# Performance work log

Hardware: AMD Instinct MI355X
Metric: run time of the kernel (lower is better)

The kernel has to match this reference:

```python
import jax, jax.numpy as jnp
import numpy as np

B, L_I, L_H, L_Q, Hs, Ws, K, A = 256, 2, 150, 10, 128, 128, 40, 5


def _conv(x, w, pad):
    # NCHW conv, stride 1
    return jax.lax.conv_general_dilated(
        x, w, window_strides=(1, 1), padding=[(pad, pad), (pad, pad)],
        dimension_numbers=('NCHW', 'OIHW', 'NCHW'))


def setup_inputs() -> dict:
    key = jax.random.key(0)
    ks = jax.random.split(key, 8)
    return {
        'input_view': jax.random.normal(ks[0], (B, L_I, Hs, Ws), dtype=jnp.float32),
        'coords': jax.random.randint(ks[1], (B, 4), 0, Hs, dtype=jnp.int32),
        'h_w': jax.random.normal(ks[2], (L_H, L_I, 3, 3), dtype=jnp.float32) * 0.05,
        'h_b': jax.random.normal(ks[3], (L_H,), dtype=jnp.float32) * 0.05,
        'r_w': jax.random.normal(ks[4], (1, L_H, 1, 1), dtype=jnp.float32) * 0.05,
        'q_w': jax.random.normal(ks[5], (L_Q, 1, 3, 3), dtype=jnp.float32) * 0.05,
        'w': jax.random.normal(ks[6], (L_Q, 1, 3, 3), dtype=jnp.float32) * 0.05,
        'fc_w': jax.random.normal(ks[7], (A, L_Q), dtype=jnp.float32) * 0.05,
    }


def reference(input_view, coords, h_w, h_b, r_w, q_w, w, fc_w):
    # process_input: h = Conv3x3(input_view), r = Conv1x1(h), q0 = Conv3x3(r)
    h = _conv(input_view, h_w, pad=1) + h_b[None, :, None, None]
    r = _conv(h, r_w, pad=0)                       # [B,1,H,W] reward map
    q = _conv(r, q_w, pad=1)                       # [B,L_Q,H,W]
    v = jnp.max(q, axis=1, keepdims=True)          # [B,1,H,W]

    # value_iteration: k-1 sweeps of eval_q + channel max, then one final eval_q
    wq = jnp.concatenate([q_w, w], axis=1)         # [L_Q,2,3,3]

    def step(_, v):
        q_i = _conv(jnp.concatenate([r, v], axis=1), wq, pad=1)
        return jnp.max(q_i, axis=1, keepdims=True)

    v = jax.lax.fori_loop(0, K - 1, step, v)
    q = _conv(jnp.concatenate([r, v], axis=1), wq, pad=1)  # [B,L_Q,H,W]

    # get_action: gather q at agent state, then fc (no bias)
    sx, sy = coords[:, 0], coords[:, 1]
    q_out = q[jnp.arange(B), :, sx, sy]            # [B,L_Q]
    logits = q_out @ fc_w.T                        # [B,5]
    return logits
```

## Files before the change

### kernel.cpp

```cpp
#include <hip/hip_runtime.h>

#define NBATCH 256
#define LI 2
#define LH 150
#define LQ 10
#define HS 128
#define WSD 128
#define KIT 40
#define AOUT 5

#define LCOLS 132
#define LROWS 130
#define PLANE (LROWS * LCOLS)
#define LDS_DWORDS (2 * PLANE)

#define WSOFF_RPLANES 64
#define WS_NEED_BYTES ((size_t)(WSOFF_RPLANES + NBATCH * PLANE) * 4)

typedef float v2f __attribute__((ext_vector_type(2)));
#define SPLAT(K) ((v2f){(K), (K)})
#define FMA2(A, B, C) __builtin_elementwise_fma((A), (B), (C))

__global__ void prep_weff(const float* __restrict__ h_w,
                          const float* __restrict__ h_b,
                          const float* __restrict__ r_w,
                          float* __restrict__ w_eff) {
  const int t = threadIdx.x;
  if (t < 18) {
    const int i = t / 9, k = t % 9;
    double s = 0.0;
    for (int h = 0; h < LH; ++h)
      s += (double)r_w[h] * (double)h_w[(h * LI + i) * 9 + k];
    w_eff[t] = (float)s;
  } else if (t == 18) {
    double s = 0.0;
    for (int h = 0; h < LH; ++h)
      s += (double)r_w[h] * (double)h_b[h];
    w_eff[18] = (float)s;
  }
}


#define LOAD_PROW(P, R, W)                                                   \
  {                                                                          \
    const float4 b_ = *reinterpret_cast<const float4*>((P) + (R) * LCOLS);   \
    const float2 c_ = *reinterpret_cast<const float2*>((P) + (R) * LCOLS + 4); \
    W[0] = (v2f){b_.x, b_.y};                                                \
    W[1] = (v2f){b_.z, b_.w};                                                \
    W[2] = (v2f){c_.x, c_.y};                                                \
  }

#define TAPROW(KY, WARR, K0, K1, K2)                                         \
    a0 = FMA2(SPLAT(K0), WARR[KY][0], a0);                                   \
    a1 = FMA2(SPLAT(K0), WARR[KY][1], a1);                                   \
    a0.x = __builtin_fmaf((K1), WARR[KY][0].y, a0.x);                        \
    a0.y = __builtin_fmaf((K1), WARR[KY][1].x, a0.y);                        \
    a1.x = __builtin_fmaf((K1), WARR[KY][1].y, a1.x);                        \
    a1.y = __builtin_fmaf((K1), WARR[KY][2].x, a1.y);                        \
    a0 = FMA2(SPLAT(K2), WARR[KY][1], a0);                                   \
    a1 = FMA2(SPLAT(K2), WARR[KY][2], a1);

#define VI_CH(QC, WC, MERGE)                                                 \
  {                                                                          \
    const float* qc = (QC);                                                  \
    const float* wc = (WC);                                                  \
    v2f a0 = SPLAT(qc[0]) * rw[0][0];                                        \
    v2f a1 = SPLAT(qc[0]) * rw[0][1];                                        \
    a0.x = __builtin_fmaf(qc[1], rw[0][0].y, a0.x);                          \
    a0.y = __builtin_fmaf(qc[1], rw[0][1].x, a0.y);                          \
    a1.x = __builtin_fmaf(qc[1], rw[0][1].y, a1.x);                          \
    a1.y = __builtin_fmaf(qc[1], rw[0][2].x, a1.y);                          \
    a0 = FMA2(SPLAT(qc[2]), rw[0][1], a0);                                   \
    a1 = FMA2(SPLAT(qc[2]), rw[0][2], a1);                                   \
    TAPROW(1, rw, qc[3], qc[4], qc[5])                                       \
    TAPROW(2, rw, qc[6], qc[7], qc[8])                                       \
    TAPROW(0, vw, wc[0], wc[1], wc[2])                                       \
    TAPROW(1, vw, wc[3], wc[4], wc[5])                                       \
    TAPROW(2, vw, wc[6], wc[7], wc[8])                                       \
    MERGE                                                                    \
  }

#define VI_CHANNELS                                                          \
    v2f o0, o1;                                                              \
    VI_CH(q_w, w_in, o0 = a0; o1 = a1;)                                      \
    _Pragma("unroll 3")                                                      \
    for (int c = 1; c < LQ; ++c) {                                           \
      VI_CH(q_w + c * 9, w_in + c * 9,                                       \
            o0 = __builtin_elementwise_max(o0, a0);                          \
            o1 = __builtin_elementwise_max(o1, a1);)                         \
    }

#define VI_ROW_L(DY)                                                         \
  {                                                                          \
    VI_CHANNELS                                                              \
    outv[DY][0] = o0; outv[DY][1] = o1;                                      \
  }

#define WIN_SHIFT2(NEXTROW)                                                  \
  {                                                                          \
    _Pragma("unroll")                                                        \
    for (int j = 0; j < 3; ++j) {                                            \
      rw[0][j] = rw[1][j]; rw[1][j] = rw[2][j];                              \
      vw[0][j] = vw[1][j]; vw[1][j] = vw[2][j];                              \
    }                                                                        \
    LOAD_PROW(rp, (NEXTROW), rw[2])                                          \
    LOAD_PROW(vp, (NEXTROW), vw[2])                                          \
  }

#define R_ROW(DY)                                                            \
  {                                                                          \
    v2f a0 = SPLAT(beff);                                                    \
    v2f a1 = a0;                                                             \
    TAPROW(0, rw, w_eff[0], w_eff[1], w_eff[2])                              \
    TAPROW(1, rw, w_eff[3], w_eff[4], w_eff[5])                              \
    TAPROW(2, rw, w_eff[6], w_eff[7], w_eff[8])                              \
    TAPROW(0, vw, w_eff[9], w_eff[10], w_eff[11])                            \
    TAPROW(1, vw, w_eff[12], w_eff[13], w_eff[14])                           \
    TAPROW(2, vw, w_eff[15], w_eff[16], w_eff[17])                           \
    racc[DY][0] = a0; racc[DY][1] = a1;                                      \
  }

#define LOADR(SLOT, R)                                                       \
  {                                                                          \
    const float4 b_ = *reinterpret_cast<const float4*>(rp + (R) * LCOLS);    \
    const float2 c_ = *reinterpret_cast<const float2*>(rp + (R) * LCOLS + 4); \
    rP[SLOT][0] = (v2f){b_.x, b_.y};                                         \
    rP[SLOT][1] = (v2f){b_.z, b_.w};                                         \
    rP[SLOT][2] = (v2f){c_.x, c_.y};                                         \
  }

#define LOADV(SLOT, R)                                                       \
  {                                                                          \
    const float4 b_ = *reinterpret_cast<const float4*>(vp + (R) * LCOLS);    \
    const float2 c_ = *reinterpret_cast<const float2*>(vp + (R) * LCOLS + 4); \
    vE[SLOT][0] = (v2f){b_.x, b_.y};                                         \
    vE[SLOT][1] = (v2f){b_.z, b_.w};                                         \
    vE[SLOT][2] = (v2f){c_.x, c_.y};                                         \
    vO[SLOT][0] = (v2f){b_.y, b_.z};                                         \
    vO[SLOT][1] = (v2f){b_.w, c_.x};                                         \
  }

#define TAP_R(SLOT, K0, K1, K2)                                              \
    a0 = FMA2(SPLAT(K0), rP[SLOT][0], a0);                                   \
    a1 = FMA2(SPLAT(K0), rP[SLOT][1], a1);                                   \
    a0.x = __builtin_fmaf((K1), rP[SLOT][0].y, a0.x);                        \
    a0.y = __builtin_fmaf((K1), rP[SLOT][1].x, a0.y);                        \
    a1.x = __builtin_fmaf((K1), rP[SLOT][1].y, a1.x);                        \
    a1.y = __builtin_fmaf((K1), rP[SLOT][2].x, a1.y);                        \
    a0 = FMA2(SPLAT(K2), rP[SLOT][1], a0);                                   \
    a1 = FMA2(SPLAT(K2), rP[SLOT][2], a1);

#define TAP_V(SLOT, K0, K1, K2)                                              \
    a0 = FMA2(SPLAT(K0), vE[SLOT][0], a0);                                   \
    a1 = FMA2(SPLAT(K0), vE[SLOT][1], a1);                                   \
    a0 = FMA2(SPLAT(K1), vO[SLOT][0], a0);                                   \
    a1 = FMA2(SPLAT(K1), vO[SLOT][1], a1);                                   \
    a0 = FMA2(SPLAT(K2), vE[SLOT][1], a0);                                   \
    a1 = FMA2(SPLAT(K2), vE[SLOT][2], a1);

#define VI_CH3(QC, WC, SA, SB, SC, MERGE)                                    \
  {                                                                          \
    const float* qc = (QC);                                                  \
    const float* wc = (WC);                                                  \
    v2f a0 = SPLAT(qc[0]) * rP[SA][0];                                       \
    v2f a1 = SPLAT(qc[0]) * rP[SA][1];                                       \
    a0.x = __builtin_fmaf(qc[1], rP[SA][0].y, a0.x);                         \
    a0.y = __builtin_fmaf(qc[1], rP[SA][1].x, a0.y);                         \
    a1.x = __builtin_fmaf(qc[1], rP[SA][1].y, a1.x);                         \
    a1.y = __builtin_fmaf(qc[1], rP[SA][2].x, a1.y);                         \
    a0 = FMA2(SPLAT(qc[2]), rP[SA][1], a0);                                  \
    a1 = FMA2(SPLAT(qc[2]), rP[SA][2], a1);                                  \
    TAP_R(SB, qc[3], qc[4], qc[5])                                           \
    TAP_R(SC, qc[6], qc[7], qc[8])                                           \
    TAP_V(SA, wc[0], wc[1], wc[2])                                           \
    TAP_V(SB, wc[3], wc[4], wc[5])                                           \
    TAP_V(SC, wc[6], wc[7], wc[8])                                           \
    MERGE                                                                    \
  }

#define VI_OUT(DY, SA, SB, SC)                                               \
  {                                                                          \
    v2f o0, o1;                                                              \
    VI_CH3(q_w, w_in, SA, SB, SC, o0 = a0; o1 = a1;)                         \
    _Pragma("unroll 3")                                                      \
    for (int c = 1; c < LQ; ++c) {                                           \
      VI_CH3(q_w + c * 9, w_in + c * 9, SA, SB, SC,                          \
             o0 = __builtin_elementwise_max(o0, a0);                         \
             o1 = __builtin_elementwise_max(o1, a1);)                        \
    }                                                                        \
    float* w_ = wr + (DY) * LCOLS;                                           \
    w_[1] = o0.x; w_[2] = o0.y; w_[3] = o1.x; w_[4] = o1.y;                  \
  }

__global__ __launch_bounds__(1024)
__attribute__((amdgpu_waves_per_eu(4, 4)))
void vin_gr(const float* __restrict__ input,
            const int* __restrict__ coords,
            const float* __restrict__ q_w,
            const float* __restrict__ w_in,
            const float* __restrict__ fc_w,
            float* __restrict__ ws,
            float* __restrict__ out) {
  extern __shared__ float lds[];
  float* pA = lds;
  float* pB = lds + PLANE;
  const float* w_eff = ws;
  float* g_r = ws + WSOFF_RPLANES + (size_t)blockIdx.x * PLANE;

  const int b = blockIdx.x;
  const int tid = threadIdx.x;
  const int ty = tid >> 5;
  const int tx = tid & 31;
  const int y0 = ty << 2;
  const int x0 = tx << 2;
  const int nb_base = y0 * LCOLS + x0;
  const int wrow0 = (y0 + 1) * LCOLS + x0;

  for (int i = tid; i < LDS_DWORDS; i += 1024) lds[i] = 0.0f;
  if (tid < LCOLS) { g_r[tid] = 0.0f; g_r[129 * LCOLS + tid] = 0.0f; }
  if (tid >= 256 && tid < 384) {
    const int row = tid - 255;
    g_r[row * LCOLS + 0] = 0.0f;
    g_r[row * LCOLS + 129] = 0.0f;
    g_r[row * LCOLS + 130] = 0.0f;
    g_r[row * LCOLS + 131] = 0.0f;
  }
  __syncthreads();

  const float* in0 = input + (size_t)b * (LI * HS * WSD);
  const float* in1 = in0 + HS * WSD;
  {
    const float4* in40 = (const float4*)in0;
    const float4* in41 = (const float4*)in1;
    for (int i = tid; i < HS * WSD / 4; i += 1024) {
      const int y = i >> 5, x4 = (i & 31) << 2;
      const float4 a = in40[i];
      const float4 c = in41[i];
      float* r_ = pA + (y + 1) * LCOLS + x4;
      float* v_ = pB + (y + 1) * LCOLS + x4;
      r_[1] = a.x; r_[2] = a.y; r_[3] = a.z; r_[4] = a.w;
      v_[1] = c.x; v_[2] = c.y; v_[3] = c.z; v_[4] = c.w;
    }
  }
  __syncthreads();

  {
    const float* rp = pA + nb_base;
    const float* vp = pB + nb_base;
    v2f rw[3][3], vw[3][3], racc[4][2];
    LOAD_PROW(rp, 0, rw[0]) LOAD_PROW(rp, 1, rw[1]) LOAD_PROW(rp, 2, rw[2])
    LOAD_PROW(vp, 0, vw[0]) LOAD_PROW(vp, 1, vw[1]) LOAD_PROW(vp, 2, vw[2])
    const float beff = w_eff[18];
    R_ROW(0) WIN_SHIFT2(3) R_ROW(1) WIN_SHIFT2(4) R_ROW(2) WIN_SHIFT2(5) R_ROW(3)
    __syncthreads();
#pragma unroll
    for (int dy = 0; dy < 4; ++dy) {
      float* g_ = g_r + wrow0 + dy * LCOLS;
      float* v_ = pA + wrow0 + dy * LCOLS;
      g_[1] = racc[dy][0].x; g_[2] = racc[dy][0].y;
      g_[3] = racc[dy][1].x; g_[4] = racc[dy][1].y;
      v_[1] = 0.0f; v_[2] = 0.0f; v_[3] = 0.0f; v_[4] = 0.0f;
    }
  }
  __syncthreads();

  const float* grp = g_r + nb_base;
#pragma unroll 1
  for (int it = 0; it < KIT; ++it) {
    const float* vp = lds + ((it & 1) ? PLANE : 0) + nb_base;
    float* wr = lds + ((it & 1) ? 0 : PLANE) + wrow0;
    const float* rp = grp;
    v2f rP[3][3], vE[3][3], vO[3][2];
    LOADR(0, 0) LOADR(1, 1) LOADR(2, 2)
    LOADV(0, 0) LOADV(1, 1) LOADV(2, 2)
    VI_OUT(0, 0, 1, 2)
    LOADR(0, 3) LOADV(0, 3)
    VI_OUT(1, 1, 2, 0)
    LOADR(1, 4) LOADV(1, 4)
    VI_OUT(2, 2, 0, 1)
    LOADR(2, 5) LOADV(2, 5)
    VI_OUT(3, 0, 1, 2)
    __syncthreads();
  }

  if (tid == 0) {
    const int sx = coords[b * 4 + 0];
    const int sy = coords[b * 4 + 1];
    float qv[LQ];
#pragma unroll 1
    for (int c = 0; c < LQ; ++c) {
      float s = 0.0f;
#pragma unroll
      for (int kk = 0; kk < 9; ++kk) {
        const int ky = kk / 3, kx = kk % 3;
        const int off = (sx + ky) * LCOLS + (sy + kx);
        s = __builtin_fmaf(q_w[c * 9 + kk], g_r[off],
            __builtin_fmaf(w_in[c * 9 + kk], pA[off], s));
      }
      qv[c] = s;
    }
#pragma unroll 1
    for (int a = 0; a < AOUT; ++a) {
      float s = 0.0f;
#pragma unroll
      for (int c = 0; c < LQ; ++c)
        s = __builtin_fmaf(fc_w[a * LQ + c], qv[c], s);
      out[b * AOUT + a] = s;
    }
  }
}

__global__ __launch_bounds__(1024)
__attribute__((amdgpu_waves_per_eu(4, 4)))
void vin_lds(const float* __restrict__ input,
             const int* __restrict__ coords,
             const float* __restrict__ q_w,
             const float* __restrict__ w_in,
             const float* __restrict__ fc_w,
             const float* __restrict__ w_eff,
             float* __restrict__ out) {
  extern __shared__ float lds[];
  float* rplane = lds;
  float* vplane = lds + PLANE;

  const int b = blockIdx.x;
  const int tid = threadIdx.x;
  const int ty = tid >> 5;
  const int tx = tid & 31;
  const int y0 = ty << 2;
  const int x0 = tx << 2;
  const int nb_base = y0 * LCOLS + x0;
  const int wrow0 = (y0 + 1) * LCOLS + x0;

  for (int i = tid; i < LDS_DWORDS; i += 1024) lds[i] = 0.0f;
  __syncthreads();

  const float* in0 = input + (size_t)b * (LI * HS * WSD);
  const float* in1 = in0 + HS * WSD;
  {
    const float4* in40 = (const float4*)in0;
    const float4* in41 = (const float4*)in1;
    for (int i = tid; i < HS * WSD / 4; i += 1024) {
      const int y = i >> 5, x4 = (i & 31) << 2;
      const float4 a = in40[i];
      const float4 c = in41[i];
      float* r_ = rplane + (y + 1) * LCOLS + x4;
      float* v_ = vplane + (y + 1) * LCOLS + x4;
      r_[1] = a.x; r_[2] = a.y; r_[3] = a.z; r_[4] = a.w;
      v_[1] = c.x; v_[2] = c.y; v_[3] = c.z; v_[4] = c.w;
    }
  }
  __syncthreads();

  {
    const float* rp = rplane + nb_base;
    const float* vp = vplane + nb_base;
    v2f rw[3][3], vw[3][3], racc[4][2];
    LOAD_PROW(rp, 0, rw[0]) LOAD_PROW(rp, 1, rw[1]) LOAD_PROW(rp, 2, rw[2])
    LOAD_PROW(vp, 0, vw[0]) LOAD_PROW(vp, 1, vw[1]) LOAD_PROW(vp, 2, vw[2])
    const float beff = w_eff[18];
    R_ROW(0) WIN_SHIFT2(3) R_ROW(1) WIN_SHIFT2(4) R_ROW(2) WIN_SHIFT2(5) R_ROW(3)
    __syncthreads();
#pragma unroll
    for (int dy = 0; dy < 4; ++dy) {
      float* r_ = rplane + wrow0 + dy * LCOLS;
      float* v_ = vplane + wrow0 + dy * LCOLS;
      r_[1] = racc[dy][0].x; r_[2] = racc[dy][0].y;
      r_[3] = racc[dy][1].x; r_[4] = racc[dy][1].y;
      v_[1] = 0.0f; v_[2] = 0.0f; v_[3] = 0.0f; v_[4] = 0.0f;
    }
  }
  __syncthreads();

#pragma unroll 1
  for (int it = 0; it < KIT; ++it) {
    const float* rp = rplane + nb_base;
    const float* vp = vplane + nb_base;
    v2f rw[3][3], vw[3][3], outv[4][2];
    LOAD_PROW(rp, 0, rw[0]) LOAD_PROW(rp, 1, rw[1]) LOAD_PROW(rp, 2, rw[2])
    LOAD_PROW(vp, 0, vw[0]) LOAD_PROW(vp, 1, vw[1]) LOAD_PROW(vp, 2, vw[2])
    VI_ROW_L(0) WIN_SHIFT2(3) VI_ROW_L(1) WIN_SHIFT2(4) VI_ROW_L(2) WIN_SHIFT2(5) VI_ROW_L(3)
    __syncthreads();
#pragma unroll
    for (int dy = 0; dy < 4; ++dy) {
      float* v_ = vplane + wrow0 + dy * LCOLS;
      v_[1] = outv[dy][0].x; v_[2] = outv[dy][0].y;
      v_[3] = outv[dy][1].x; v_[4] = outv[dy][1].y;
    }
    __syncthreads();
  }

  if (tid == 0) {
    const int sx = coords[b * 4 + 0];
    const int sy = coords[b * 4 + 1];
    float qv[LQ];
#pragma unroll 1
    for (int c = 0; c < LQ; ++c) {
      float s = 0.0f;
#pragma unroll
      for (int kk = 0; kk < 9; ++kk) {
        const int ky = kk / 3, kx = kk % 3;
        const int off = (sx + ky) * LCOLS + (sy + kx);
        s = __builtin_fmaf(q_w[c * 9 + kk], rplane[off],
            __builtin_fmaf(w_in[c * 9 + kk], vplane[off], s));
      }
      qv[c] = s;
    }
#pragma unroll 1
    for (int a = 0; a < AOUT; ++a) {
      float s = 0.0f;
#pragma unroll
      for (int c = 0; c < LQ; ++c)
        s = __builtin_fmaf(fc_w[a * LQ + c], qv[c], s);
      out[b * AOUT + a] = s;
    }
  }
}

extern "C" void kernel_launch(void* const* d_in, const int* in_sizes, int n_in,
                              void* d_out, int out_size, void* d_ws, size_t ws_size,
                              hipStream_t stream) {
  const float* input = (const float*)d_in[0];
  const int*   coords = (const int*)d_in[1];
  const float* h_w = (const float*)d_in[2];
  const float* h_b = (const float*)d_in[3];
  const float* r_w = (const float*)d_in[4];
  const float* q_w = (const float*)d_in[5];
  const float* w_in = (const float*)d_in[6];
  const float* fc_w = (const float*)d_in[7];
  float* out = (float*)d_out;
  float* ws = (float*)d_ws;

  const size_t smem = (size_t)LDS_DWORDS * sizeof(float);

  prep_weff<<<1, 64, 0, stream>>>(h_w, h_b, r_w, ws);

  if (ws_size >= WS_NEED_BYTES) {
    hipFuncSetAttribute(reinterpret_cast<const void*>(vin_gr),
                        hipFuncAttributeMaxDynamicSharedMemorySize, (int)smem);
    vin_gr<<<NBATCH, 1024, smem, stream>>>(input, coords, q_w, w_in, fc_w, ws, out);
  } else {
    hipFuncSetAttribute(reinterpret_cast<const void*>(vin_lds),
                        hipFuncAttributeMaxDynamicSharedMemorySize, (int)smem);
    vin_lds<<<NBATCH, 1024, smem, stream>>>(input, coords, q_w, w_in, fc_w, ws, out);
  }
}
```

Baseline: 664.3 us.

## Precompute per-channel reward-conv terms once and stream them from workspace each sweep

Adds a vin_rq kernel that computes the q_w 3x3 convolution of the reward map for all 10 Q channels once and writes it to a per-batch global workspace buffer. Each value-iteration sweep then loads these precomputed terms as float4 and only convolves the value plane with w, instead of recomputing the reward-side convolution every iteration. This roughly halves the per-sweep FMA work. In exchange it adds about 167 MB of workspace traffic that is re-read on every one of the 39 sweeps, which may exceed cache capacity and make the kernel bandwidth-bound. The new path is used only when the provided workspace is large enough; otherwise the previous kernels still run.

```diff
diff --git a/kernel.cpp b/kernel.cpp
--- a/kernel.cpp
+++ b/kernel.cpp
@@ -16,6 +16,9 @@
 
 #define WSOFF_RPLANES 64
 #define WS_NEED_BYTES ((size_t)(WSOFF_RPLANES + NBATCH * PLANE) * 4)
+#define WSOFF_RQ 64
+#define RQPLANE (HS * LQ * WSD)
+#define WS_RQ_BYTES ((size_t)(WSOFF_RQ + (size_t)NBATCH * RQPLANE) * 4)
 
 typedef float v2f __attribute__((ext_vector_type(2)));
 #define SPLAT(K) ((v2f){(K), (K)})
@@ -192,6 +195,212 @@
     w_[1] = o0.x; w_[2] = o0.y; w_[3] = o1.x; w_[4] = o1.y;                  \
   }
 
+#define RQ_CH3(QC, SA, SB, SC, MERGE)                                        \
+  {                                                                          \
+    const float* qc = (QC);                                                  \
+    v2f a0 = SPLAT(qc[0]) * rP[SA][0];                                       \
+    v2f a1 = SPLAT(qc[0]) * rP[SA][1];                                       \
+    a0.x = __builtin_fmaf(qc[1], rP[SA][0].y, a0.x);                         \
+    a0.y = __builtin_fmaf(qc[1], rP[SA][1].x, a0.y);                         \
+    a1.x = __builtin_fmaf(qc[1], rP[SA][1].y, a1.x);                         \
+    a1.y = __builtin_fmaf(qc[1], rP[SA][2].x, a1.y);                         \
+    a0 = FMA2(SPLAT(qc[2]), rP[SA][1], a0);                                  \
+    a1 = FMA2(SPLAT(qc[2]), rP[SA][2], a1);                                  \
+    TAP_R(SB, qc[3], qc[4], qc[5])                                           \
+    TAP_R(SC, qc[6], qc[7], qc[8])                                           \
+    MERGE                                                                    \
+  }
+
+#define RQ_ST(CI)                                                            \
+    *reinterpret_cast<float4*>(sr + (CI) * WSD) =                            \
+        make_float4(a0.x, a0.y, a1.x, a1.y);
+
+#define RQ_MX                                                                \
+    m0 = __builtin_elementwise_max(m0, a0);                                  \
+    m1 = __builtin_elementwise_max(m1, a1);
+
+#define RQ_OUT(DY, SA, SB, SC)                                               \
+  {                                                                          \
+    float* sr = rq_t + (DY) * (LQ * WSD);                                    \
+    v2f m0, m1;                                                              \
+    RQ_CH3(q_w + 0,  SA, SB, SC, RQ_ST(0) m0 = a0; m1 = a1;)                 \
+    RQ_CH3(q_w + 9,  SA, SB, SC, RQ_ST(1) RQ_MX)                             \
+    RQ_CH3(q_w + 18, SA, SB, SC, RQ_ST(2) RQ_MX)                             \
+    RQ_CH3(q_w + 27, SA, SB, SC, RQ_ST(3) RQ_MX)                             \
+    RQ_CH3(q_w + 36, SA, SB, SC, RQ_ST(4) RQ_MX)                             \
+    RQ_CH3(q_w + 45, SA, SB, SC, RQ_ST(5) RQ_MX)                             \
+    RQ_CH3(q_w + 54, SA, SB, SC, RQ_ST(6) RQ_MX)                             \
+    RQ_CH3(q_w + 63, SA, SB, SC, RQ_ST(7) RQ_MX)                             \
+    RQ_CH3(q_w + 72, SA, SB, SC, RQ_ST(8) RQ_MX)                             \
+    RQ_CH3(q_w + 81, SA, SB, SC, RQ_ST(9) RQ_MX)                             \
+    float* v_ = vwr + (DY) * LCOLS;                                          \
+    v_[1] = m0.x; v_[2] = m0.y; v_[3] = m1.x; v_[4] = m1.y;                  \
+  }
+
+#define VI_CHV(Q4, WOFF, SA, SB, SC, MERGE)                                  \
+  {                                                                          \
+    const float* wc = w_in + (WOFF);                                         \
+    v2f a0 = (v2f){(Q4).x, (Q4).y};                                          \
+    v2f a1 = (v2f){(Q4).z, (Q4).w};                                          \
+    TAP_V(SA, wc[0], wc[1], wc[2])                                           \
+    TAP_V(SB, wc[3], wc[4], wc[5])                                           \
+    TAP_V(SC, wc[6], wc[7], wc[8])                                           \
+    MERGE                                                                    \
+  }
+
+#define VI_MXO                                                               \
+    o0 = __builtin_elementwise_max(o0, a0);                                  \
+    o1 = __builtin_elementwise_max(o1, a1);
+
+#define VI_OUT_RQ(DY, SA, SB, SC)                                            \
+  {                                                                          \
+    const float* rqr = rq_t + (DY) * (LQ * WSD);                             \
+    const float4 q0 = *reinterpret_cast<const float4*>(rqr + 0 * WSD);       \
+    const float4 q1 = *reinterpret_cast<const float4*>(rqr + 1 * WSD);       \
+    const float4 q2 = *reinterpret_cast<const float4*>(rqr + 2 * WSD);       \
+    const float4 q3 = *reinterpret_cast<const float4*>(rqr + 3 * WSD);       \
+    const float4 q4 = *reinterpret_cast<const float4*>(rqr + 4 * WSD);       \
+    const float4 q5 = *reinterpret_cast<const float4*>(rqr + 5 * WSD);       \
+    const float4 q6 = *reinterpret_cast<const float4*>(rqr + 6 * WSD);       \
+    const float4 q7 = *reinterpret_cast<const float4*>(rqr + 7 * WSD);       \
+    const float4 q8 = *reinterpret_cast<const float4*>(rqr + 8 * WSD);       \
+    const float4 q9 = *reinterpret_cast<const float4*>(rqr + 9 * WSD);       \
+    v2f o0, o1;                                                              \
+    VI_CHV(q0,  0, SA, SB, SC, o0 = a0; o1 = a1;)                            \
+    VI_CHV(q1,  9, SA, SB, SC, VI_MXO)                                       \
+    VI_CHV(q2, 18, SA, SB, SC, VI_MXO)                                       \
+    VI_CHV(q3, 27, SA, SB, SC, VI_MXO)                                       \
+    VI_CHV(q4, 36, SA, SB, SC, VI_MXO)                                       \
+    VI_CHV(q5, 45, SA, SB, SC, VI_MXO)                                       \
+    VI_CHV(q6, 54, SA, SB, SC, VI_MXO)                                       \
+    VI_CHV(q7, 63, SA, SB, SC, VI_MXO)                                       \
+    VI_CHV(q8, 72, SA, SB, SC, VI_MXO)                                       \
+    VI_CHV(q9, 81, SA, SB, SC, VI_MXO)                                       \
+    float* w_ = wr + (DY) * LCOLS;                                           \
+    w_[1] = o0.x; w_[2] = o0.y; w_[3] = o1.x; w_[4] = o1.y;                  \
+  }
+
+__global__ __launch_bounds__(1024)
+__attribute__((amdgpu_waves_per_eu(4, 4)))
+void vin_rq(const float* __restrict__ input,
+            const int* __restrict__ coords,
+            const float* __restrict__ q_w,
+            const float* __restrict__ w_in,
+            const float* __restrict__ fc_w,
+            float* __restrict__ ws,
+            float* __restrict__ out) {
+  extern __shared__ float lds[];
+  float* pA = lds;
+  float* pB = lds + PLANE;
+  const float* w_eff = ws;
+
+  const int b = blockIdx.x;
+  const int tid = threadIdx.x;
+  const int ty = tid >> 5;
+  const int tx = tid & 31;
+  const int y0 = ty << 2;
+  const int x0 = tx << 2;
+  const int nb_base = y0 * LCOLS + x0;
+  const int wrow0 = (y0 + 1) * LCOLS + x0;
+
+  float* rq_t = ws + WSOFF_RQ + (size_t)b * RQPLANE + (y0 * LQ) * WSD + x0;
+
+  for (int i = tid; i < LDS_DWORDS; i += 1024) lds[i] = 0.0f;
+  __syncthreads();
+
+  const float* in0 = input + (size_t)b * (LI * HS * WSD);
+  const float* in1 = in0 + HS * WSD;
+  {
+    const float4* in40 = (const float4*)in0;
+    const float4* in41 = (const float4*)in1;
+    for (int i = tid; i < HS * WSD / 4; i += 1024) {
+      const int y = i >> 5, x4 = (i & 31) << 2;
+      const float4 a = in40[i];
+      const float4 c = in41[i];
+      float* r_ = pA + (y + 1) * LCOLS + x4;
+      float* v_ = pB + (y + 1) * LCOLS + x4;
+      r_[1] = a.x; r_[2] = a.y; r_[3] = a.z; r_[4] = a.w;
+      v_[1] = c.x; v_[2] = c.y; v_[3] = c.z; v_[4] = c.w;
+    }
+  }
+  __syncthreads();
+
+  {
+    const float* rp = pA + nb_base;
+    const float* vp = pB + nb_base;
+    v2f rw[3][3], vw[3][3], racc[4][2];
+    LOAD_PROW(rp, 0, rw[0]) LOAD_PROW(rp, 1, rw[1]) LOAD_PROW(rp, 2, rw[2])
+    LOAD_PROW(vp, 0, vw[0]) LOAD_PROW(vp, 1, vw[1]) LOAD_PROW(vp, 2, vw[2])
+    const float beff = w_eff[18];
+    R_ROW(0) WIN_SHIFT2(3) R_ROW(1) WIN_SHIFT2(4) R_ROW(2) WIN_SHIFT2(5) R_ROW(3)
+    __syncthreads();
+#pragma unroll
+    for (int dy = 0; dy < 4; ++dy) {
+      float* r_ = pA + wrow0 + dy * LCOLS;
+      r_[1] = racc[dy][0].x; r_[2] = racc[dy][0].y;
+      r_[3] = racc[dy][1].x; r_[4] = racc[dy][1].y;
+    }
+  }
+  __syncthreads();
+
+  {
+    const float* rp = pA + nb_base;
+    float* vwr = pB + wrow0;
+    v2f rP[3][3];
+    LOADR(0, 0) LOADR(1, 1) LOADR(2, 2)
+    RQ_OUT(0, 0, 1, 2)
+    LOADR(0, 3)
+    RQ_OUT(1, 1, 2, 0)
+    LOADR(1, 4)
+    RQ_OUT(2, 2, 0, 1)
+    LOADR(2, 5)
+    RQ_OUT(3, 0, 1, 2)
+  }
+  __syncthreads();
+
+#pragma unroll 1
+  for (int it = 0; it < KIT - 1; ++it) {
+    const float* vp = lds + ((it & 1) ? 0 : PLANE) + nb_base;
+    float* wr = lds + ((it & 1) ? PLANE : 0) + wrow0;
+    v2f vE[3][3], vO[3][2];
+    LOADV(0, 0) LOADV(1, 1) LOADV(2, 2)
+    VI_OUT_RQ(0, 0, 1, 2)
+    LOADV(0, 3)
+    VI_OUT_RQ(1, 1, 2, 0)
+    LOADV(1, 4)
+    VI_OUT_RQ(2, 2, 0, 1)
+    LOADV(2, 5)
+    VI_OUT_RQ(3, 0, 1, 2)
+    __syncthreads();
+  }
+
+  if (tid == 0) {
+    const int sx = coords[b * 4 + 0];
+    const int sy = coords[b * 4 + 1];
+    const float* rq_b = ws + WSOFF_RQ + (size_t)b * RQPLANE;
+    float qv[LQ];
+#pragma unroll 1
+    for (int c = 0; c < LQ; ++c) {
+      float s = rq_b[(sx * LQ + c) * WSD + sy];
+#pragma unroll
+      for (int kk = 0; kk < 9; ++kk) {
+        const int ky = kk / 3, kx = kk % 3;
+        const int off = (sx + ky) * LCOLS + (sy + kx);
+        s = __builtin_fmaf(w_in[c * 9 + kk], pA[off], s);
+      }
+      qv[c] = s;
+    }
+#pragma unroll 1
+    for (int a = 0; a < AOUT; ++a) {
+      float s = 0.0f;
+#pragma unroll
+      for (int c = 0; c < LQ; ++c)
+        s = __builtin_fmaf(fc_w[a * LQ + c], qv[c], s);
+      out[b * AOUT + a] = s;
+    }
+  }
+}
+
 __global__ __launch_bounds__(1024)
 __attribute__((amdgpu_waves_per_eu(4, 4)))
 void vin_gr(const float* __restrict__ input,
@@ -435,7 +644,11 @@
 
   prep_weff<<<1, 64, 0, stream>>>(h_w, h_b, r_w, ws);
 
-  if (ws_size >= WS_NEED_BYTES) {
+  if (ws_size >= WS_RQ_BYTES) {
+    hipFuncSetAttribute(reinterpret_cast<const void*>(vin_rq),
+                        hipFuncAttributeMaxDynamicSharedMemorySize, (int)smem);
+    vin_rq<<<NBATCH, 1024, smem, stream>>>(input, coords, q_w, w_in, fc_w, ws, out);
+  } else if (ws_size >= WS_NEED_BYTES) {
     hipFuncSetAttribute(reinterpret_cast<const void*>(vin_gr),
                         hipFuncAttributeMaxDynamicSharedMemorySize, (int)smem);
     vin_gr<<<NBATCH, 1024, smem, stream>>>(input, coords, q_w, w_in, fc_w, ws, out);
```

After: 1.126 ms. 1.69x slower.

## Peel initial q0 step and cache r-conv for two channels in registers

Applied to the files above, without the earlier changes.

Replaces vin_gr with vin_rr. It computes the initial q=conv(r,q_w) and channel max explicitly and writes v into LDS, which removes one full value-iteration sweep (the loop now runs K-1 times instead of K). The r-contributions of channels 0 and 1 are cached in registers (rqA/rqB), since r is constant across iterations, so those channels skip the r-taps each sweep. It also adds odd-shifted r registers (rO) so the r-taps use packed FMA instead of scalar FMAs. The cost is more register pressure under the fixed 4-waves-per-EU bound, which risks spills.

```diff
diff --git a/kernel.cpp b/kernel.cpp
--- a/kernel.cpp
+++ b/kernel.cpp
@@ -60,6 +60,308 @@
     a0 = FMA2(SPLAT(K2), WARR[KY][1], a0);                                   \
     a1 = FMA2(SPLAT(K2), WARR[KY][2], a1);
 
+#define WIN_SHIFT2(NEXTROW)                                                  \
+  {                                                                          \
+    _Pragma("unroll")                                                        \
+    for (int j = 0; j < 3; ++j) {                                            \
+      rw[0][j] = rw[1][j]; rw[1][j] = rw[2][j];                              \
+      vw[0][j] = vw[1][j]; vw[1][j] = vw[2][j];                              \
+    }                                                                        \
+    LOAD_PROW(rp, (NEXTROW), rw[2])                                          \
+    LOAD_PROW(vp, (NEXTROW), vw[2])                                          \
+  }
+
+#define R_ROW(DY)                                                            \
+  {                                                                          \
+    v2f a0 = SPLAT(beff);                                                    \
+    v2f a1 = a0;                                                             \
+    TAPROW(0, rw, w_eff[0], w_eff[1], w_eff[2])                              \
+    TAPROW(1, rw, w_eff[3], w_eff[4], w_eff[5])                              \
+    TAPROW(2, rw, w_eff[6], w_eff[7], w_eff[8])                              \
+    TAPROW(0, vw, w_eff[9], w_eff[10], w_eff[11])                            \
+    TAPROW(1, vw, w_eff[12], w_eff[13], w_eff[14])                           \
+    TAPROW(2, vw, w_eff[15], w_eff[16], w_eff[17])                           \
+    racc[DY][0] = a0; racc[DY][1] = a1;                                      \
+  }
+
+#define LOADR(SLOT, R)                                                       \
+  {                                                                          \
+    const float4 b_ = *reinterpret_cast<const float4*>(rp + (R) * LCOLS);    \
+    const float2 c_ = *reinterpret_cast<const float2*>(rp + (R) * LCOLS + 4); \
+    rP[SLOT][0] = (v2f){b_.x, b_.y};                                         \
+    rP[SLOT][1] = (v2f){b_.z, b_.w};                                         \
+    rP[SLOT][2] = (v2f){c_.x, c_.y};                                         \
+  }
+
+#define LOADR2(SLOT, R)                                                      \
+  {                                                                          \
+    const float4 b_ = *reinterpret_cast<const float4*>(rp + (R) * LCOLS);    \
+    const float2 c_ = *reinterpret_cast<const float2*>(rp + (R) * LCOLS + 4); \
+    rP[SLOT][0] = (v2f){b_.x, b_.y};                                         \
+    rP[SLOT][1] = (v2f){b_.z, b_.w};                                         \
+    rP[SLOT][2] = (v2f){c_.x, c_.y};                                         \
+    rO[SLOT][0] = (v2f){b_.y, b_.z};                                         \
+    rO[SLOT][1] = (v2f){b_.w, c_.x};                                         \
+  }
+
+#define LOADV(SLOT, R)                                                       \
+  {                                                                          \
+    const float4 b_ = *reinterpret_cast<const float4*>(vp + (R) * LCOLS);    \
+    const float2 c_ = *reinterpret_cast<const float2*>(vp + (R) * LCOLS + 4); \
+    vE[SLOT][0] = (v2f){b_.x, b_.y};                                         \
+    vE[SLOT][1] = (v2f){b_.z, b_.w};                                         \
+    vE[SLOT][2] = (v2f){c_.x, c_.y};                                         \
+    vO[SLOT][0] = (v2f){b_.y, b_.z};                                         \
+    vO[SLOT][1] = (v2f){b_.w, c_.x};                                         \
+  }
+
+#define TAP_R(SLOT, K0, K1, K2)                                              \
+    a0 = FMA2(SPLAT(K0), rP[SLOT][0], a0);                                   \
+    a1 = FMA2(SPLAT(K0), rP[SLOT][1], a1);                                   \
+    a0.x = __builtin_fmaf((K1), rP[SLOT][0].y, a0.x);                        \
+    a0.y = __builtin_fmaf((K1), rP[SLOT][1].x, a0.y);                        \
+    a1.x = __builtin_fmaf((K1), rP[SLOT][1].y, a1.x);                        \
+    a1.y = __builtin_fmaf((K1), rP[SLOT][2].x, a1.y);                        \
+    a0 = FMA2(SPLAT(K2), rP[SLOT][1], a0);                                   \
+    a1 = FMA2(SPLAT(K2), rP[SLOT][2], a1);
+
+#define TAP_R2(SLOT, K0, K1, K2)                                             \
+    a0 = FMA2(SPLAT(K0), rP[SLOT][0], a0);                                   \
+    a1 = FMA2(SPLAT(K0), rP[SLOT][1], a1);                                   \
+    a0 = FMA2(SPLAT(K1), rO[SLOT][0], a0);                                   \
+    a1 = FMA2(SPLAT(K1), rO[SLOT][1], a1);                                   \
+    a0 = FMA2(SPLAT(K2), rP[SLOT][1], a0);                                   \
+    a1 = FMA2(SPLAT(K2), rP[SLOT][2], a1);
+
+#define TAP_V(SLOT, K0, K1, K2)                                              \
+    a0 = FMA2(SPLAT(K0), vE[SLOT][0], a0);                                   \
+    a1 = FMA2(SPLAT(K0), vE[SLOT][1], a1);                                   \
+    a0 = FMA2(SPLAT(K1), vO[SLOT][0], a0);                                   \
+    a1 = FMA2(SPLAT(K1), vO[SLOT][1], a1);                                   \
+    a0 = FMA2(SPLAT(K2), vE[SLOT][1], a0);                                   \
+    a1 = FMA2(SPLAT(K2), vE[SLOT][2], a1);
+
+#define RQ_CH3(QC, SA, SB, SC, MERGE)                                        \
+  {                                                                          \
+    const float* qc = (QC);                                                  \
+    v2f a0 = SPLAT(qc[0]) * rP[SA][0];                                       \
+    v2f a1 = SPLAT(qc[0]) * rP[SA][1];                                       \
+    a0.x = __builtin_fmaf(qc[1], rP[SA][0].y, a0.x);                         \
+    a0.y = __builtin_fmaf(qc[1], rP[SA][1].x, a0.y);                         \
+    a1.x = __builtin_fmaf(qc[1], rP[SA][1].y, a1.x);                         \
+    a1.y = __builtin_fmaf(qc[1], rP[SA][2].x, a1.y);                         \
+    a0 = FMA2(SPLAT(qc[2]), rP[SA][1], a0);                                  \
+    a1 = FMA2(SPLAT(qc[2]), rP[SA][2], a1);                                  \
+    TAP_R(SB, qc[3], qc[4], qc[5])                                           \
+    TAP_R(SC, qc[6], qc[7], qc[8])                                           \
+    MERGE                                                                    \
+  }
+
+#define RQ_MX                                                                \
+    m0 = __builtin_elementwise_max(m0, a0);                                  \
+    m1 = __builtin_elementwise_max(m1, a1);
+
+#define RQ_OUT11(DY, SA, SB, SC)                                             \
+  {                                                                          \
+    v2f m0, m1;                                                              \
+    RQ_CH3(q_w + 0,  SA, SB, SC,                                             \
+           rqA[DY][0] = a0; rqA[DY][1] = a1; m0 = a0; m1 = a1;)              \
+    RQ_CH3(q_w + 9,  SA, SB, SC,                                             \
+           rqB[DY][0] = a0; rqB[DY][1] = a1; RQ_MX)                          \
+    RQ_CH3(q_w + 18, SA, SB, SC, RQ_MX)                                      \
+    RQ_CH3(q_w + 27, SA, SB, SC, RQ_MX)                                      \
+    RQ_CH3(q_w + 36, SA, SB, SC, RQ_MX)                                      \
+    RQ_CH3(q_w + 45, SA, SB, SC, RQ_MX)                                      \
+    RQ_CH3(q_w + 54, SA, SB, SC, RQ_MX)                                      \
+    RQ_CH3(q_w + 63, SA, SB, SC, RQ_MX)                                      \
+    RQ_CH3(q_w + 72, SA, SB, SC, RQ_MX)                                      \
+    RQ_CH3(q_w + 81, SA, SB, SC, RQ_MX)                                      \
+    float* v_ = vwr + (DY) * LCOLS;                                          \
+    v_[1] = m0.x; v_[2] = m0.y; v_[3] = m1.x; v_[4] = m1.y;                  \
+  }
+
+#define VI_CHR(RQ0, RQ1, WOFF, SA, SB, SC, MERGE)                            \
+  {                                                                          \
+    const float* wc = w_in + (WOFF);                                         \
+    v2f a0 = (RQ0);                                                          \
+    v2f a1 = (RQ1);                                                          \
+    TAP_V(SA, wc[0], wc[1], wc[2])                                           \
+    TAP_V(SB, wc[3], wc[4], wc[5])                                           \
+    TAP_V(SC, wc[6], wc[7], wc[8])                                           \
+    MERGE                                                                    \
+  }
+
+#define VI_CHF(QC, WC, SA, SB, SC, MERGE)                                    \
+  {                                                                          \
+    const float* qc = (QC);                                                  \
+    const float* wc = (WC);                                                  \
+    v2f a0 = SPLAT(qc[0]) * rP[SA][0];                                       \
+    v2f a1 = SPLAT(qc[0]) * rP[SA][1];                                       \
+    a0 = FMA2(SPLAT(qc[1]), rO[SA][0], a0);                                  \
+    a1 = FMA2(SPLAT(qc[1]), rO[SA][1], a1);                                  \
+    a0 = FMA2(SPLAT(qc[2]), rP[SA][1], a0);                                  \
+    a1 = FMA2(SPLAT(qc[2]), rP[SA][2], a1);                                  \
+    TAP_R2(SB, qc[3], qc[4], qc[5])                                          \
+    TAP_R2(SC, qc[6], qc[7], qc[8])                                          \
+    TAP_V(SA, wc[0], wc[1], wc[2])                                           \
+    TAP_V(SB, wc[3], wc[4], wc[5])                                           \
+    TAP_V(SC, wc[6], wc[7], wc[8])                                           \
+    MERGE                                                                    \
+  }
+
+#define VI_MXO                                                               \
+    o0 = __builtin_elementwise_max(o0, a0);                                  \
+    o1 = __builtin_elementwise_max(o1, a1);
+
+#define VI_OUT11(DY, SA, SB, SC)                                             \
+  {                                                                          \
+    v2f o0, o1;                                                              \
+    VI_CHR(rqA[DY][0], rqA[DY][1], 0, SA, SB, SC, o0 = a0; o1 = a1;)         \
+    VI_CHR(rqB[DY][0], rqB[DY][1], 9, SA, SB, SC, VI_MXO)                    \
+    _Pragma("unroll")                                                        \
+    for (int c = 2; c < LQ; ++c) {                                           \
+      VI_CHF(q_w + c * 9, w_in + c * 9, SA, SB, SC, VI_MXO)                  \
+    }                                                                        \
+    float* w_ = wr + (DY) * LCOLS;                                           \
+    w_[1] = o0.x; w_[2] = o0.y; w_[3] = o1.x; w_[4] = o1.y;                  \
+  }
+
+__global__ __launch_bounds__(1024)
+__attribute__((amdgpu_waves_per_eu(4, 4)))
+void vin_rr(const float* __restrict__ input,
+            const int* __restrict__ coords,
+            const float* __restrict__ q_w,
+            const float* __restrict__ w_in,
+            const float* __restrict__ fc_w,
+            float* __restrict__ ws,
+            float* __restrict__ out) {
+  extern __shared__ float lds[];
+  float* pA = lds;
+  float* pB = lds + PLANE;
+  const float* w_eff = ws;
+  float* g_r = ws + WSOFF_RPLANES + (size_t)blockIdx.x * PLANE;
+
+  const int b = blockIdx.x;
+  const int tid = threadIdx.x;
+  const int ty = tid >> 5;
+  const int tx = tid & 31;
+  const int y0 = ty << 2;
+  const int x0 = tx << 2;
+  const int nb_base = y0 * LCOLS + x0;
+  const int wrow0 = (y0 + 1) * LCOLS + x0;
+
+  v2f rqA[4][2], rqB[4][2];
+
+  for (int i = tid; i < LDS_DWORDS; i += 1024) lds[i] = 0.0f;
+  if (tid < LCOLS) { g_r[tid] = 0.0f; g_r[129 * LCOLS + tid] = 0.0f; }
+  if (tid >= 256 && tid < 384) {
+    const int row = tid - 255;
+    g_r[row * LCOLS + 0] = 0.0f;
+    g_r[row * LCOLS + 129] = 0.0f;
+    g_r[row * LCOLS + 130] = 0.0f;
+    g_r[row * LCOLS + 131] = 0.0f;
+  }
+  __syncthreads();
+
+  const float* in0 = input + (size_t)b * (LI * HS * WSD);
+  const float* in1 = in0 + HS * WSD;
+  {
+    const float4* in40 = (const float4*)in0;
+    const float4* in41 = (const float4*)in1;
+    for (int i = tid; i < HS * WSD / 4; i += 1024) {
+      const int y = i >> 5, x4 = (i & 31) << 2;
+      const float4 a = in40[i];
+      const float4 c = in41[i];
+      float* r_ = pA + (y + 1) * LCOLS + x4;
+      float* v_ = pB + (y + 1) * LCOLS + x4;
+      r_[1] = a.x; r_[2] = a.y; r_[3] = a.z; r_[4] = a.w;
+      v_[1] = c.x; v_[2] = c.y; v_[3] = c.z; v_[4] = c.w;
+    }
+  }
+  __syncthreads();
+
+  {
+    const float* rp = pA + nb_base;
+    const float* vp = pB + nb_base;
+    v2f rw[3][3], vw[3][3], racc[4][2];
+    LOAD_PROW(rp, 0, rw[0]) LOAD_PROW(rp, 1, rw[1]) LOAD_PROW(rp, 2, rw[2])
+    LOAD_PROW(vp, 0, vw[0]) LOAD_PROW(vp, 1, vw[1]) LOAD_PROW(vp, 2, vw[2])
+    const float beff = w_eff[18];
+    R_ROW(0) WIN_SHIFT2(3) R_ROW(1) WIN_SHIFT2(4) R_ROW(2) WIN_SHIFT2(5) R_ROW(3)
+    __syncthreads();
+#pragma unroll
+    for (int dy = 0; dy < 4; ++dy) {
+      float* g_ = g_r + wrow0 + dy * LCOLS;
+      float* r_ = pA + wrow0 + dy * LCOLS;
+      g_[1] = racc[dy][0].x; g_[2] = racc[dy][0].y;
+      g_[3] = racc[dy][1].x; g_[4] = racc[dy][1].y;
+      r_[1] = racc[dy][0].x; r_[2] = racc[dy][0].y;
+      r_[3] = racc[dy][1].x; r_[4] = racc[dy][1].y;
+    }
+  }
+  __syncthreads();
+
+  {
+    const float* rp = pA + nb_base;
+    float* vwr = pB + wrow0;
+    v2f rP[3][3];
+    LOADR(0, 0) LOADR(1, 1) LOADR(2, 2)
+    RQ_OUT11(0, 0, 1, 2)
+    LOADR(0, 3)
+    RQ_OUT11(1, 1, 2, 0)
+    LOADR(1, 4)
+    RQ_OUT11(2, 2, 0, 1)
+    LOADR(2, 5)
+    RQ_OUT11(3, 0, 1, 2)
+  }
+  __syncthreads();
+
+  const float* grp = g_r + nb_base;
+#pragma unroll 1
+  for (int it = 0; it < KIT - 1; ++it) {
+    const float* vp = lds + ((it & 1) ? 0 : PLANE) + nb_base;
+    float* wr = lds + ((it & 1) ? PLANE : 0) + wrow0;
+    const float* rp = grp;
+    v2f rP[3][3], rO[3][2], vE[3][3], vO[3][2];
+    LOADR2(0, 0) LOADR2(1, 1) LOADR2(2, 2)
+    LOADV(0, 0) LOADV(1, 1) LOADV(2, 2)
+    VI_OUT11(0, 0, 1, 2)
+    LOADR2(0, 3) LOADV(0, 3)
+    VI_OUT11(1, 1, 2, 0)
+    LOADR2(1, 4) LOADV(1, 4)
+    VI_OUT11(2, 2, 0, 1)
+    LOADR2(2, 5) LOADV(2, 5)
+    VI_OUT11(3, 0, 1, 2)
+    __syncthreads();
+  }
+
+  if (tid == 0) {
+    const int sx = coords[b * 4 + 0];
+    const int sy = coords[b * 4 + 1];
+    float qv[LQ];
+#pragma unroll 1
+    for (int c = 0; c < LQ; ++c) {
+      float s = 0.0f;
+#pragma unroll
+      for (int kk = 0; kk < 9; ++kk) {
+        const int ky = kk / 3, kx = kk % 3;
+        const int off = (sx + ky) * LCOLS + (sy + kx);
+        s = __builtin_fmaf(q_w[c * 9 + kk], g_r[off],
+            __builtin_fmaf(w_in[c * 9 + kk], pA[off], s));
+      }
+      qv[c] = s;
+    }
+#pragma unroll 1
+    for (int a = 0; a < AOUT; ++a) {
+      float s = 0.0f;
+#pragma unroll
+      for (int c = 0; c < LQ; ++c)
+        s = __builtin_fmaf(fc_w[a * LQ + c], qv[c], s);
+      out[b * AOUT + a] = s;
+    }
+  }
+}
+
 #define VI_CH(QC, WC, MERGE)                                                 \
   {                                                                          \
     const float* qc = (QC);                                                  \
@@ -80,7 +382,8 @@
     MERGE                                                                    \
   }
 
-#define VI_CHANNELS                                                          \
+#define VI_ROW_L(DY)                                                         \
+  {                                                                          \
     v2f o0, o1;                                                              \
     VI_CH(q_w, w_in, o0 = a0; o1 = a1;)                                      \
     _Pragma("unroll 3")                                                      \
@@ -88,227 +391,9 @@
       VI_CH(q_w + c * 9, w_in + c * 9,                                       \
             o0 = __builtin_elementwise_max(o0, a0);                          \
             o1 = __builtin_elementwise_max(o1, a1);)                         \
-    }
-
-#define VI_ROW_L(DY)                                                         \
-  {                                                                          \
-    VI_CHANNELS                                                              \
+    }                                                                        \
     outv[DY][0] = o0; outv[DY][1] = o1;                                      \
   }
-
-#define WIN_SHIFT2(NEXTROW)                                                  \
-  {                                                                          \
-    _Pragma("unroll")                                                        \
-    for (int j = 0; j < 3; ++j) {                                            \
-      rw[0][j] = rw[1][j]; rw[1][j] = rw[2][j];                              \
-      vw[0][j] = vw[1][j]; vw[1][j] = vw[2][j];                              \
-    }                                                                        \
-    LOAD_PROW(rp, (NEXTROW), rw[2])                                          \
-    LOAD_PROW(vp, (NEXTROW), vw[2])                                          \
-  }
-
-#define R_ROW(DY)                                                            \
-  {                                                                          \
-    v2f a0 = SPLAT(beff);                                                    \
-    v2f a1 = a0;                                                             \
-    TAPROW(0, rw, w_eff[0], w_eff[1], w_eff[2])                              \
-    TAPROW(1, rw, w_eff[3], w_eff[4], w_eff[5])                              \
-    TAPROW(2, rw, w_eff[6], w_eff[7], w_eff[8])                              \
-    TAPROW(0, vw, w_eff[9], w_eff[10], w_eff[11])                            \
-    TAPROW(1, vw, w_eff[12], w_eff[13], w_eff[14])                           \
-    TAPROW(2, vw, w_eff[15], w_eff[16], w_eff[17])                           \
-    racc[DY][0] = a0; racc[DY][1] = a1;                                      \
-  }
-
-#define LOADR(SLOT, R)                                                       \
-  {                                                                          \
-    const float4 b_ = *reinterpret_cast<const float4*>(rp + (R) * LCOLS);    \
-    const float2 c_ = *reinterpret_cast<const float2*>(rp + (R) * LCOLS + 4); \
-    rP[SLOT][0] = (v2f){b_.x, b_.y};                                         \
-    rP[SLOT][1] = (v2f){b_.z, b_.w};                                         \
-    rP[SLOT][2] = (v2f){c_.x, c_.y};                                         \
-  }
-
-#define LOADV(SLOT, R)                                                       \
-  {                                                                          \
-    const float4 b_ = *reinterpret_cast<const float4*>(vp + (R) * LCOLS);    \
-    const float2 c_ = *reinterpret_cast<const float2*>(vp + (R) * LCOLS + 4); \
-    vE[SLOT][0] = (v2f){b_.x, b_.y};                                         \
-    vE[SLOT][1] = (v2f){b_.z, b_.w};                                         \
-    vE[SLOT][2] = (v2f){c_.x, c_.y};                                         \
-    vO[SLOT][0] = (v2f){b_.y, b_.z};                                         \
-    vO[SLOT][1] = (v2f){b_.w, c_.x};                                         \
-  }
-
-#define TAP_R(SLOT, K0, K1, K2)                                              \
-    a0 = FMA2(SPLAT(K0), rP[SLOT][0], a0);                                   \
-    a1 = FMA2(SPLAT(K0), rP[SLOT][1], a1);                                   \
-    a0.x = __builtin_fmaf((K1), rP[SLOT][0].y, a0.x);                        \
-    a0.y = __builtin_fmaf((K1), rP[SLOT][1].x, a0.y);                        \
-    a1.x = __builtin_fmaf((K1), rP[SLOT][1].y, a1.x);                        \
-    a1.y = __builtin_fmaf((K1), rP[SLOT][2].x, a1.y);                        \
-    a0 = FMA2(SPLAT(K2), rP[SLOT][1], a0);                                   \
-    a1 = FMA2(SPLAT(K2), rP[SLOT][2], a1);
-
-#define TAP_V(SLOT, K0, K1, K2)                                              \
-    a0 = FMA2(SPLAT(K0), vE[SLOT][0], a0);                                   \
-    a1 = FMA2(SPLAT(K0), vE[SLOT][1], a1);                                   \
-    a0 = FMA2(SPLAT(K1), vO[SLOT][0], a0);                                   \
-    a1 = FMA2(SPLAT(K1), vO[SLOT][1], a1);                                   \
-    a0 = FMA2(SPLAT(K2), vE[SLOT][1], a0);                                   \
-    a1 = FMA2(SPLAT(K2), vE[SLOT][2], a1);
-
-#define VI_CH3(QC, WC, SA, SB, SC, MERGE)                                    \
-  {                                                                          \
-    const float* qc = (QC);                                                  \
-    const float* wc = (WC);                                                  \
-    v2f a0 = SPLAT(qc[0]) * rP[SA][0];                                       \
-    v2f a1 = SPLAT(qc[0]) * rP[SA][1];                                       \
-    a0.x = __builtin_fmaf(qc[1], rP[SA][0].y, a0.x);                         \
-    a0.y = __builtin_fmaf(qc[1], rP[SA][1].x, a0.y);                         \
-    a1.x = __builtin_fmaf(qc[1], rP[SA][1].y, a1.x);                         \
-    a1.y = __builtin_fmaf(qc[1], rP[SA][2].x, a1.y);                         \
-    a0 = FMA2(SPLAT(qc[2]), rP[SA][1], a0);                                  \
-    a1 = FMA2(SPLAT(qc[2]), rP[SA][2], a1);                                  \
-    TAP_R(SB, qc[3], qc[4], qc[5])                                           \
-    TAP_R(SC, qc[6], qc[7], qc[8])                                           \
-    TAP_V(SA, wc[0], wc[1], wc[2])                                           \
-    TAP_V(SB, wc[3], wc[4], wc[5])                                           \
-    TAP_V(SC, wc[6], wc[7], wc[8])                                           \
-    MERGE                                                                    \
-  }
-
-#define VI_OUT(DY, SA, SB, SC)                                               \
-  {                                                                          \
-    v2f o0, o1;                                                              \
-    VI_CH3(q_w, w_in, SA, SB, SC, o0 = a0; o1 = a1;)                         \
-    _Pragma("unroll 3")                                                      \
-    for (int c = 1; c < LQ; ++c) {                                           \
-      VI_CH3(q_w + c * 9, w_in + c * 9, SA, SB, SC,                          \
-             o0 = __builtin_elementwise_max(o0, a0);                         \
-             o1 = __builtin_elementwise_max(o1, a1);)                        \
-    }                                                                        \
-    float* w_ = wr + (DY) * LCOLS;                                           \
-    w_[1] = o0.x; w_[2] = o0.y; w_[3] = o1.x; w_[4] = o1.y;                  \
-  }
-
-__global__ __launch_bounds__(1024)
-__attribute__((amdgpu_waves_per_eu(4, 4)))
-void vin_gr(const float* __restrict__ input,
-            const int* __restrict__ coords,
-            const float* __restrict__ q_w,
-            const float* __restrict__ w_in,
-            const float* __restrict__ fc_w,
-            float* __restrict__ ws,
-            float* __restrict__ out) {
-  extern __shared__ float lds[];
-  float* pA = lds;
-  float* pB = lds + PLANE;
-  const float* w_eff = ws;
-  float* g_r = ws + WSOFF_RPLANES + (size_t)blockIdx.x * PLANE;
-
-  const int b = blockIdx.x;
-  const int tid = threadIdx.x;
-  const int ty = tid >> 5;
-  const int tx = tid & 31;
-  const int y0 = ty << 2;
-  const int x0 = tx << 2;
-  const int nb_base = y0 * LCOLS + x0;
-  const int wrow0 = (y0 + 1) * LCOLS + x0;
-
-  for (int i = tid; i < LDS_DWORDS; i += 1024) lds[i] = 0.0f;
-  if (tid < LCOLS) { g_r[tid] = 0.0f; g_r[129 * LCOLS + tid] = 0.0f; }
-  if (tid >= 256 && tid < 384) {
-    const int row = tid - 255;
-    g_r[row * LCOLS + 0] = 0.0f;
-    g_r[row * LCOLS + 129] = 0.0f;
-    g_r[row * LCOLS + 130] = 0.0f;
-    g_r[row * LCOLS + 131] = 0.0f;
-  }
-  __syncthreads();
-
-  const float* in0 = input + (size_t)b * (LI * HS * WSD);
-  const float* in1 = in0 + HS * WSD;
-  {
-    const float4* in40 = (const float4*)in0;
-    const float4* in41 = (const float4*)in1;
-    for (int i = tid; i < HS * WSD / 4; i += 1024) {
-      const int y = i >> 5, x4 = (i & 31) << 2;
-      const float4 a = in40[i];
-      const float4 c = in41[i];
-      float* r_ = pA + (y + 1) * LCOLS + x4;
-      float* v_ = pB + (y + 1) * LCOLS + x4;
-      r_[1] = a.x; r_[2] = a.y; r_[3] = a.z; r_[4] = a.w;
-      v_[1] = c.x; v_[2] = c.y; v_[3] = c.z; v_[4] = c.w;
-    }
-  }
-  __syncthreads();
-
-  {
-    const float* rp = pA + nb_base;
-    const float* vp = pB + nb_base;
-    v2f rw[3][3], vw[3][3], racc[4][2];
-    LOAD_PROW(rp, 0, rw[0]) LOAD_PROW(rp, 1, rw[1]) LOAD_PROW(rp, 2, rw[2])
-    LOAD_PROW(vp, 0, vw[0]) LOAD_PROW(vp, 1, vw[1]) LOAD_PROW(vp, 2, vw[2])
-    const float beff = w_eff[18];
-    R_ROW(0) WIN_SHIFT2(3) R_ROW(1) WIN_SHIFT2(4) R_ROW(2) WIN_SHIFT2(5) R_ROW(3)
-    __syncthreads();
-#pragma unroll
-    for (int dy = 0; dy < 4; ++dy) {
-      float* g_ = g_r + wrow0 + dy * LCOLS;
-      float* v_ = pA + wrow0 + dy * LCOLS;
-      g_[1] = racc[dy][0].x; g_[2] = racc[dy][0].y;
-      g_[3] = racc[dy][1].x; g_[4] = racc[dy][1].y;
-      v_[1] = 0.0f; v_[2] = 0.0f; v_[3] = 0.0f; v_[4] = 0.0f;
-    }
-  }
-  __syncthreads();
-
-  const float* grp = g_r + nb_base;
-#pragma unroll 1
-  for (int it = 0; it < KIT; ++it) {
-    const float* vp = lds + ((it & 1) ? PLANE : 0) + nb_base;
-    float* wr = lds + ((it & 1) ? 0 : PLANE) + wrow0;
-    const float* rp = grp;
-    v2f rP[3][3], vE[3][3], vO[3][2];
-    LOADR(0, 0) LOADR(1, 1) LOADR(2, 2)
-    LOADV(0, 0) LOADV(1, 1) LOADV(2, 2)
-    VI_OUT(0, 0, 1, 2)
-    LOADR(0, 3) LOADV(0, 3)
-    VI_OUT(1, 1, 2, 0)
-    LOADR(1, 4) LOADV(1, 4)
-    VI_OUT(2, 2, 0, 1)
-    LOADR(2, 5) LOADV(2, 5)
-    VI_OUT(3, 0, 1, 2)
-    __syncthreads();
-  }
-
-  if (tid == 0) {
-    const int sx = coords[b * 4 + 0];
-    const int sy = coords[b * 4 + 1];
-    float qv[LQ];
-#pragma unroll 1
-    for (int c = 0; c < LQ; ++c) {
-      float s = 0.0f;
-#pragma unroll
-      for (int kk = 0; kk < 9; ++kk) {
-        const int ky = kk / 3, kx = kk % 3;
-        const int off = (sx + ky) * LCOLS + (sy + kx);
-        s = __builtin_fmaf(q_w[c * 9 + kk], g_r[off],
-            __builtin_fmaf(w_in[c * 9 + kk], pA[off], s));
-      }
-      qv[c] = s;
-    }
-#pragma unroll 1
-    for (int a = 0; a < AOUT; ++a) {
-      float s = 0.0f;
-#pragma unroll
-      for (int c = 0; c < LQ; ++c)
-        s = __builtin_fmaf(fc_w[a * LQ + c], qv[c], s);
-      out[b * AOUT + a] = s;
-    }
-  }
-}
 
 __global__ __launch_bounds__(1024)
 __attribute__((amdgpu_waves_per_eu(4, 4)))
@@ -436,9 +521,9 @@
   prep_weff<<<1, 64, 0, stream>>>(h_w, h_b, r_w, ws);
 
   if (ws_size >= WS_NEED_BYTES) {
-    hipFuncSetAttribute(reinterpret_cast<const void*>(vin_gr),
+    hipFuncSetAttribute(reinterpret_cast<const void*>(vin_rr),
                         hipFuncAttributeMaxDynamicSharedMemorySize, (int)smem);
-    vin_gr<<<NBATCH, 1024, smem, stream>>>(input, coords, q_w, w_in, fc_w, ws, out);
+    vin_rr<<<NBATCH, 1024, smem, stream>>>(input, coords, q_w, w_in, fc_w, ws, out);
   } else {
     hipFuncSetAttribute(reinterpret_cast<const void*>(vin_lds),
                         hipFuncAttributeMaxDynamicSharedMemorySize, (int)smem);
```

After: 848.7 us. 1.28x slower.
